# Kernel optimization log

Measured on AMD Instinct MI355X. Metric: run time of the kernel, lower is better.

Reference implementation:

```python
import jax, jax.numpy as jnp
import numpy as np

Q = 128          # number of slices
S = 1024 // Q    # slice length = 8
U = 32           # hidden units per slice
EPS = 1e-3       # keras LayerNormalization default epsilon


def setup_inputs() -> dict:
    key = jax.random.key(0)
    ks = jax.random.split(key, 8)
    B = 16384
    x = jax.random.normal(ks[0], (B, 1, 1, Q * S), dtype=jnp.float32)
    # per-slice Dense1 (S->U), LayerNorm(gamma,beta), Dense2 (U->1)
    W1 = jax.random.normal(ks[1], (Q, S, U), dtype=jnp.float32) / np.sqrt(S)
    b1 = jnp.zeros((Q, U), dtype=jnp.float32)
    gamma = jnp.ones((Q, U), dtype=jnp.float32)
    beta = jnp.zeros((Q, U), dtype=jnp.float32)
    W2 = jax.random.normal(ks[2], (Q, U), dtype=jnp.float32) / np.sqrt(U)
    b2 = jnp.zeros((Q,), dtype=jnp.float32)
    return {"x": x, "W1": W1, "b1": b1, "gamma": gamma, "beta": beta,
            "W2": W2, "b2": b2}


def reference(x, W1, b1, gamma, beta, W2, b2):
    B = x.shape[0]
    xs = x.reshape(B, Q, S)                              # (B,Q,S)
    # batched tiny Dense -> ELU
    h = jnp.einsum('bqs,qsu->bqu', xs, W1) + b1          # (B,Q,U)
    h = jax.nn.elu(h)
    # per-slice LayerNorm over last axis
    mu = jnp.mean(h, axis=-1, keepdims=True)
    var = jnp.mean(jnp.square(h - mu), axis=-1, keepdims=True)
    h = (h - mu) * jax.lax.rsqrt(var + EPS) * gamma + beta
    # batched output projection U -> 1, concat over slices
    out = jnp.einsum('bqu,qu->bq', h, W2) + b2           # (B,Q)
    return out
```

## Files before the change

kernel.cpp:

```cpp
#include <hip/hip_runtime.h>


typedef __attribute__((ext_vector_type(8))) short short8;
typedef __attribute__((ext_vector_type(16))) float f32x16;

__device__ __forceinline__ short fbits(__bf16 b) { return __builtin_bit_cast(short, b); }

__device__ __forceinline__ float elu1(float v) {
    return v > 0.f ? v : __expf(v) - 1.f;
}

__global__ __launch_bounds__(256, 4) void divenc_mfma(
    const float* __restrict__ x,
    const float* __restrict__ W1,
    const float* __restrict__ b1,
    const float* __restrict__ gamma,
    const float* __restrict__ beta,
    const float* __restrict__ W2,
    const float* __restrict__ b2,
    float* __restrict__ out)
{
    __shared__ float lout[2][64 * 5];

    const int tid  = threadIdx.x;
    const int w    = tid >> 6;
    const int ln   = tid & 63;
    const int u    = ln & 31;
    const int half = ln >> 5;
    const int qt   = blockIdx.y;
    const int q    = qt * 4 + w;
    const int bx   = blockIdx.x;

    short8 wfrag;
    #pragma unroll
    for (int j = 0; j < 8; ++j) {
        float f  = W1[q * 256 + j * 32 + u];
        __bf16 h = (__bf16)f;
        wfrag[j] = half ? fbits((__bf16)(f - (float)h)) : fbits(h);
    }

    f32x16 biasr, g2r;
    float G, C;
    {
        float gs = 0.f, cs = 0.f;
        #pragma unroll
        for (int c = 0; c < 4; ++c) {
            const int ub = q * 32 + 4 * half + 8 * c;
            float4 b1v = *(const float4*)&b1[ub];
            float4 gav = *(const float4*)&gamma[ub];
            float4 w2v = *(const float4*)&W2[ub];
            float4 bev = *(const float4*)&beta[ub];
            #pragma unroll
            for (int j = 0; j < 4; ++j) {
                float g2 = ((const float*)&gav)[j] * ((const float*)&w2v)[j];
                biasr[4 * c + j] = ((const float*)&b1v)[j];
                g2r[4 * c + j]   = g2;
                gs += g2;
                cs += ((const float*)&bev)[j] * ((const float*)&w2v)[j];
            }
        }
        gs += __shfl_xor(gs, 32);
        cs += __shfl_xor(cs, 32);
        G = gs;
        C = cs + b2[q];
    }

    const float* xq = x + q * 8;

    float4 c00, c01, c10, c11;
    {
        const float* p0 = xq + (size_t)(bx * 256 + u) * 1024;
        const float* p1 = xq + (size_t)(bx * 256 + 32 + u) * 1024;
        c00 = ((const float4*)p0)[0]; c01 = ((const float4*)p0)[1];
        c10 = ((const float4*)p1)[0]; c11 = ((const float4*)p1)[1];
    }

    #pragma unroll 1
    for (int it = 0; it < 4; ++it) {
        const int b0 = bx * 256 + it * 64;

        const int bn = (it < 3) ? b0 + 64 : b0;
        const float* pn0 = xq + (size_t)(bn + u) * 1024;
        const float* pn1 = xq + (size_t)(bn + 32 + u) * 1024;
        float4 n00 = ((const float4*)pn0)[0], n01 = ((const float4*)pn0)[1];
        float4 n10 = ((const float4*)pn1)[0], n11 = ((const float4*)pn1)[1];

        float xf0[8] = {c00.x, c00.y, c00.z, c00.w, c01.x, c01.y, c01.z, c01.w};
        float xf1[8] = {c10.x, c10.y, c10.z, c10.w, c11.x, c11.y, c11.z, c11.w};
        short8 xa, xb;
        #pragma unroll
        for (int j = 0; j < 8; ++j) {
            xa[j] = fbits((__bf16)xf0[j]);
            xb[j] = fbits((__bf16)xf1[j]);
        }

        f32x16 acc0 = __builtin_amdgcn_mfma_f32_32x32x16_bf16(wfrag, xa, biasr, 0, 0, 0);
        f32x16 acc1 = __builtin_amdgcn_mfma_f32_32x32x16_bf16(wfrag, xb, biasr, 0, 0, 0);

        float res0, res1;
        {
            float sum = 0.f, ss = 0.f, dot = 0.f;
            #pragma unroll
            for (int r = 0; r < 16; ++r) {
                float e = elu1(acc0[r]);
                sum += e;
                ss  = fmaf(e, e, ss);
                dot = fmaf(e, g2r[r], dot);
            }
            sum += __shfl_xor(sum, 32);
            ss  += __shfl_xor(ss, 32);
            dot += __shfl_xor(dot, 32);
            float mu  = sum * 0.03125f;
            float var = fmaf(-mu, mu, ss * 0.03125f);
            float inv = rsqrtf(var + 1e-3f);
            res0 = fmaf(inv, fmaf(-mu, G, dot), C);
        }
        {
            float sum = 0.f, ss = 0.f, dot = 0.f;
            #pragma unroll
            for (int r = 0; r < 16; ++r) {
                float e = elu1(acc1[r]);
                sum += e;
                ss  = fmaf(e, e, ss);
                dot = fmaf(e, g2r[r], dot);
            }
            sum += __shfl_xor(sum, 32);
            ss  += __shfl_xor(ss, 32);
            dot += __shfl_xor(dot, 32);
            float mu  = sum * 0.03125f;
            float var = fmaf(-mu, mu, ss * 0.03125f);
            float inv = rsqrtf(var + 1e-3f);
            res1 = fmaf(inv, fmaf(-mu, G, dot), C);
        }

        if (half == 0) {
            lout[it & 1][u * 5 + w]        = res0;
            lout[it & 1][(u + 32) * 5 + w] = res1;
        }
        __syncthreads();

        if (tid < 64) {
            const float* lb = lout[it & 1];
            float4 o;
            o.x = lb[tid * 5 + 0];
            o.y = lb[tid * 5 + 1];
            o.z = lb[tid * 5 + 2];
            o.w = lb[tid * 5 + 3];
            *(float4*)(out + (size_t)(b0 + tid) * 128 + qt * 4) = o;
        }

        c00 = n00; c01 = n01; c10 = n10; c11 = n11;
    }
}

extern "C" void kernel_launch(void* const* d_in, const int* in_sizes, int n_in,
                              void* d_out, int out_size, void* d_ws, size_t ws_size,
                              hipStream_t stream) {
    const float* x     = (const float*)d_in[0];
    const float* W1    = (const float*)d_in[1];
    const float* b1    = (const float*)d_in[2];
    const float* gamma = (const float*)d_in[3];
    const float* beta  = (const float*)d_in[4];
    const float* W2    = (const float*)d_in[5];
    const float* b2    = (const float*)d_in[6];
    float* out = (float*)d_out;

    dim3 grid(64, 32);
    divenc_mfma<<<grid, 256, 0, stream>>>(x, W1, b1, gamma, beta, W2, b2, out);
}
```

Baseline: 31.29 us.

## Stage x panels into LDS with async global_load_lds and a single output store

Instead of each wave loading its own 32-byte slices from global memory per iteration, all 256 threads issue direct global-to-LDS loads of four 64-row x 128-byte panels up front. A swizzled layout spreads LDS banks, and staged vmcnt waits let compute on one panel overlap the loads still in flight. Outputs go into one LDS buffer and are written with a single coalesced store at the end instead of four barrier-separated stores. This adds LDS use (about 37 KB per block), which may limit occupancy, and relies on hand-written waitcnt/barrier asm for correctness.

```diff
diff --git a/kernel.cpp b/kernel.cpp
--- a/kernel.cpp
+++ b/kernel.cpp
@@ -10,7 +10,70 @@
     return v > 0.f ? v : __expf(v) - 1.f;
 }
 
-__global__ __launch_bounds__(256, 4) void divenc_mfma(
+__device__ __forceinline__ void compute_panel(
+    const float* __restrict__ pan, int b0, short8 wfrag,
+    const f32x16& biasr, const f32x16& g2r, float G, float C,
+    int u, int w, int half, float* __restrict__ lout)
+{
+    const int s0 = 4 * ((2 * w) ^ (u & 7));
+    const int s1 = 4 * ((2 * w + 1) ^ (u & 7));
+    float4 a0 = *(const float4*)&pan[u * 32 + s0];
+    float4 a1 = *(const float4*)&pan[u * 32 + s1];
+    float4 c0 = *(const float4*)&pan[1024 + u * 32 + s0];
+    float4 c1 = *(const float4*)&pan[1024 + u * 32 + s1];
+
+    short8 xa, xb;
+    xa[0] = fbits((__bf16)a0.x); xa[1] = fbits((__bf16)a0.y);
+    xa[2] = fbits((__bf16)a0.z); xa[3] = fbits((__bf16)a0.w);
+    xa[4] = fbits((__bf16)a1.x); xa[5] = fbits((__bf16)a1.y);
+    xa[6] = fbits((__bf16)a1.z); xa[7] = fbits((__bf16)a1.w);
+    xb[0] = fbits((__bf16)c0.x); xb[1] = fbits((__bf16)c0.y);
+    xb[2] = fbits((__bf16)c0.z); xb[3] = fbits((__bf16)c0.w);
+    xb[4] = fbits((__bf16)c1.x); xb[5] = fbits((__bf16)c1.y);
+    xb[6] = fbits((__bf16)c1.z); xb[7] = fbits((__bf16)c1.w);
+
+    f32x16 accA = __builtin_amdgcn_mfma_f32_32x32x16_bf16(wfrag, xa, biasr, 0, 0, 0);
+    f32x16 accB = __builtin_amdgcn_mfma_f32_32x32x16_bf16(wfrag, xb, biasr, 0, 0, 0);
+
+    {
+        float sum = 0.f, ss = 0.f, dot = 0.f;
+        #pragma unroll
+        for (int r = 0; r < 16; ++r) {
+            float e = elu1(accA[r]);
+            sum += e;
+            ss  = fmaf(e, e, ss);
+            dot = fmaf(e, g2r[r], dot);
+        }
+        sum += __shfl_xor(sum, 32);
+        ss  += __shfl_xor(ss, 32);
+        dot += __shfl_xor(dot, 32);
+        float mu  = sum * 0.03125f;
+        float var = fmaf(-mu, mu, ss * 0.03125f);
+        float inv = rsqrtf(var + 1e-3f);
+        float res = fmaf(inv, fmaf(-mu, G, dot), C);
+        if (half == 0) lout[(b0 + u) * 5 + w] = res;
+    }
+    {
+        float sum = 0.f, ss = 0.f, dot = 0.f;
+        #pragma unroll
+        for (int r = 0; r < 16; ++r) {
+            float e = elu1(accB[r]);
+            sum += e;
+            ss  = fmaf(e, e, ss);
+            dot = fmaf(e, g2r[r], dot);
+        }
+        sum += __shfl_xor(sum, 32);
+        ss  += __shfl_xor(ss, 32);
+        dot += __shfl_xor(dot, 32);
+        float mu  = sum * 0.03125f;
+        float var = fmaf(-mu, mu, ss * 0.03125f);
+        float inv = rsqrtf(var + 1e-3f);
+        float res = fmaf(inv, fmaf(-mu, G, dot), C);
+        if (half == 0) lout[(b0 + 32 + u) * 5 + w] = res;
+    }
+}
+
+__global__ __launch_bounds__(256, 4) void divenc_dp(
     const float* __restrict__ x,
     const float* __restrict__ W1,
     const float* __restrict__ b1,
@@ -20,7 +83,8 @@
     const float* __restrict__ b2,
     float* __restrict__ out)
 {
-    __shared__ float lout[2][64 * 5];
+    __shared__ float xp[4][64 * 32];
+    __shared__ float lout[256 * 5];
 
     const int tid  = threadIdx.x;
     const int w    = tid >> 6;
@@ -30,6 +94,7 @@
     const int qt   = blockIdx.y;
     const int q    = qt * 4 + w;
     const int bx   = blockIdx.x;
+    const int band = bx * 256;
 
     short8 wfrag;
     #pragma unroll
@@ -65,91 +130,39 @@
         C = cs + b2[q];
     }
 
-    const float* xq = x + q * 8;
-
-    float4 c00, c01, c10, c11;
     {
-        const float* p0 = xq + (size_t)(bx * 256 + u) * 1024;
-        const float* p1 = xq + (size_t)(bx * 256 + 32 + u) * 1024;
-        c00 = ((const float4*)p0)[0]; c01 = ((const float4*)p0)[1];
-        c10 = ((const float4*)p1)[0]; c11 = ((const float4*)p1)[1];
+        const int rsub = ln >> 3;
+        const int chk  = (ln & 7) ^ rsub;
+        const float* gsrc = x + qt * 32 + chk * 4;
+        #pragma unroll
+        for (int p = 0; p < 4; ++p) {
+            #pragma unroll
+            for (int i = 0; i < 2; ++i) {
+                const float* ga = gsrc + (size_t)(band + p * 64 + w * 16 + i * 8 + rsub) * 1024;
+                float* la = &xp[p][(w * 16 + i * 8) * 32];
+                __builtin_amdgcn_global_load_lds(ga, la, 16, 0, 0);
+            }
+        }
     }
 
-    #pragma unroll 1
-    for (int it = 0; it < 4; ++it) {
-        const int b0 = bx * 256 + it * 64;
+    asm volatile("s_waitcnt vmcnt(6)\n\ts_barrier" ::: "memory");
+    compute_panel(&xp[0][0],   0, wfrag, biasr, g2r, G, C, u, w, half, lout);
+    asm volatile("s_waitcnt vmcnt(4)\n\ts_barrier" ::: "memory");
+    compute_panel(&xp[1][0],  64, wfrag, biasr, g2r, G, C, u, w, half, lout);
+    asm volatile("s_waitcnt vmcnt(2)\n\ts_barrier" ::: "memory");
+    compute_panel(&xp[2][0], 128, wfrag, biasr, g2r, G, C, u, w, half, lout);
+    asm volatile("s_waitcnt vmcnt(0)\n\ts_barrier" ::: "memory");
+    compute_panel(&xp[3][0], 192, wfrag, biasr, g2r, G, C, u, w, half, lout);
 
-        const int bn = (it < 3) ? b0 + 64 : b0;
-        const float* pn0 = xq + (size_t)(bn + u) * 1024;
-        const float* pn1 = xq + (size_t)(bn + 32 + u) * 1024;
-        float4 n00 = ((const float4*)pn0)[0], n01 = ((const float4*)pn0)[1];
-        float4 n10 = ((const float4*)pn1)[0], n11 = ((const float4*)pn1)[1];
+    __syncthreads();
 
-        float xf0[8] = {c00.x, c00.y, c00.z, c00.w, c01.x, c01.y, c01.z, c01.w};
-        float xf1[8] = {c10.x, c10.y, c10.z, c10.w, c11.x, c11.y, c11.z, c11.w};
-        short8 xa, xb;
-        #pragma unroll
-        for (int j = 0; j < 8; ++j) {
-            xa[j] = fbits((__bf16)xf0[j]);
-            xb[j] = fbits((__bf16)xf1[j]);
-        }
-
-        f32x16 acc0 = __builtin_amdgcn_mfma_f32_32x32x16_bf16(wfrag, xa, biasr, 0, 0, 0);
-        f32x16 acc1 = __builtin_amdgcn_mfma_f32_32x32x16_bf16(wfrag, xb, biasr, 0, 0, 0);
-
-        float res0, res1;
-        {
-            float sum = 0.f, ss = 0.f, dot = 0.f;
-            #pragma unroll
-            for (int r = 0; r < 16; ++r) {
-                float e = elu1(acc0[r]);
-                sum += e;
-                ss  = fmaf(e, e, ss);
-                dot = fmaf(e, g2r[r], dot);
-            }
-            sum += __shfl_xor(sum, 32);
-            ss  += __shfl_xor(ss, 32);
-            dot += __shfl_xor(dot, 32);
-            float mu  = sum * 0.03125f;
-            float var = fmaf(-mu, mu, ss * 0.03125f);
-            float inv = rsqrtf(var + 1e-3f);
-            res0 = fmaf(inv, fmaf(-mu, G, dot), C);
-        }
-        {
-            float sum = 0.f, ss = 0.f, dot = 0.f;
-            #pragma unroll
-            for (int r = 0; r < 16; ++r) {
-                float e = elu1(acc1[r]);
-                sum += e;
-                ss  = fmaf(e, e, ss);
-                dot = fmaf(e, g2r[r], dot);
-            }
-            sum += __shfl_xor(sum, 32);
-            ss  += __shfl_xor(ss, 32);
-            dot += __shfl_xor(dot, 32);
-            float mu  = sum * 0.03125f;
-            float var = fmaf(-mu, mu, ss * 0.03125f);
-            float inv = rsqrtf(var + 1e-3f);
-            res1 = fmaf(inv, fmaf(-mu, G, dot), C);
-        }
-
-        if (half == 0) {
-            lout[it & 1][u * 5 + w]        = res0;
-            lout[it & 1][(u + 32) * 5 + w] = res1;
-        }
-        __syncthreads();
-
-        if (tid < 64) {
-            const float* lb = lout[it & 1];
-            float4 o;
-            o.x = lb[tid * 5 + 0];
-            o.y = lb[tid * 5 + 1];
-            o.z = lb[tid * 5 + 2];
-            o.w = lb[tid * 5 + 3];
-            *(float4*)(out + (size_t)(b0 + tid) * 128 + qt * 4) = o;
-        }
-
-        c00 = n00; c01 = n01; c10 = n10; c11 = n11;
+    {
+        float4 o;
+        o.x = lout[tid * 5 + 0];
+        o.y = lout[tid * 5 + 1];
+        o.z = lout[tid * 5 + 2];
+        o.w = lout[tid * 5 + 3];
+        *(float4*)(out + (size_t)(band + tid) * 128 + qt * 4) = o;
     }
 }
 
@@ -166,5 +179,5 @@
     float* out = (float*)d_out;
 
     dim3 grid(64, 32);
-    divenc_mfma<<<grid, 256, 0, stream>>>(x, W1, b1, gamma, beta, W2, b2, out);
+    divenc_dp<<<grid, 256, 0, stream>>>(x, W1, b1, gamma, beta, W2, b2, out);
 }
```

New measurement: 28.05 us. -10.3%, faster.
